# Performance work log

Measured on AMD Instinct MI355X. Metric: run time of the kernel, lower is better.

## Reference

```python
import jax, jax.numpy as jnp
import numpy as np

BATCH = 250
SEQ = 200
EMB = 100
VOCAB = 100000
UNITS = 512


def setup_inputs() -> dict:
    key = jax.random.key(0)
    ks = jax.random.split(key, 12)
    s = 0.05
    return {
        "tokens": jax.random.randint(ks[0], (BATCH, SEQ), 0, VOCAB, dtype=jnp.int64 if jax.config.jax_enable_x64 else jnp.int32),
        "emb": jax.random.normal(ks[1], (VOCAB, EMB), jnp.float32) * s,
        "k0": jax.random.normal(ks[2], (EMB, 4 * UNITS), jnp.float32) * s,
        "r0": jax.random.normal(ks[3], (UNITS, 4 * UNITS), jnp.float32) * s,
        "b0": jnp.zeros((4 * UNITS,), jnp.float32),
        "k1": jax.random.normal(ks[4], (UNITS, 4 * UNITS), jnp.float32) * s,
        "r1": jax.random.normal(ks[5], (UNITS, 4 * UNITS), jnp.float32) * s,
        "b1": jnp.zeros((4 * UNITS,), jnp.float32),
        "wd1": jax.random.normal(ks[6], (UNITS, 32), jnp.float32) * s,
        "bd1": jnp.zeros((32,), jnp.float32),
        "wd2": jax.random.normal(ks[7], (32, 1), jnp.float32) * s,
        "bd2": jnp.zeros((1,), jnp.float32),
    }


def _lstm_step(x, h, c, k, r, b):
    # Keras LSTMCell gate order: [i, f, cbar, o]
    g = x @ k + h @ r + b  # [B, 4U]
    i, f, cbar, o = jnp.split(g, 4, axis=-1)
    c_new = jax.nn.sigmoid(f) * c + jax.nn.sigmoid(i) * jnp.tanh(cbar)
    h_new = jax.nn.sigmoid(o) * jnp.tanh(c_new)
    return h_new, c_new


def reference(tokens, emb, k0, r0, b0, k1, r1, b1, wd1, bd1, wd2, bd2):
    x = emb[tokens]  # [B, T, E]
    B = x.shape[0]
    U = r0.shape[0]

    def step(carry, xt):
        h0, c0, h1, c1 = carry
        h0, c0 = _lstm_step(xt, h0, c0, k0, r0, b0)
        h1, c1 = _lstm_step(h0, h1, c1, k1, r1, b1)
        return (h0, c0, h1, c1), None

    init = tuple(jnp.zeros((B, U), x.dtype) for _ in range(4))
    (h0, c0, h1, c1), _ = jax.lax.scan(step, init, jnp.swapaxes(x, 0, 1))
    prob = jax.nn.sigmoid((h1 @ wd1 + bd1) @ wd2 + bd2)  # [B, 1]
    return prob
```

## Files before the change

kernel.cpp:

```cpp
#include <hip/hip_runtime.h>
#include <cstdint>

typedef unsigned short u16;
typedef unsigned long long u64;
typedef __attribute__((ext_vector_type(8))) short s8v;
typedef __attribute__((ext_vector_type(4))) float f4v;

#define NBLK 256
#define TSEQ 200
#define PIPE_W 8
#define HSLOT (256 * 512)

__device__ __forceinline__ u16 f2bf(float f) {
  uint32_t u = __float_as_uint(f);
  u += 0x7fffu + ((u >> 16) & 1u);
  return (u16)(u >> 16);
}
__device__ __forceinline__ float bf2f(u16 h) {
  return __uint_as_float(((uint32_t)h) << 16);
}
__device__ __forceinline__ float sigf(float x) { return 1.f / (1.f + __expf(-x)); }
__device__ __forceinline__ float tanhfast(float x) { return 2.f / (1.f + __expf(-2.f * x)) - 1.f; }

__device__ __forceinline__ void ld_c(s8v& d, const u16* p, int ofs) {
  asm volatile("global_load_dwordx4 %0, %1, off offset:%2 sc0 sc1"
               : "=v"(d) : "v"(p), "n"(ofs));
}
__device__ __forceinline__ void ld_nc(s8v& d, const u16* p, int ofs) {
  asm volatile("global_load_dwordx4 %0, %1, off offset:%2"
               : "=v"(d) : "v"(p), "n"(ofs));
}
__device__ __forceinline__ void vmwait(int n) {
  asm volatile("s_waitcnt vmcnt(%0)" :: "n"(n) : "memory");
}
__device__ __forceinline__ void cstore(u16* p, u16 v) {
  asm volatile("global_store_short %0, %1, off sc0 sc1" :: "v"(p), "v"((uint32_t)v) : "memory");
}


__global__ void zero_ws(uint32_t* p, int n) {
  int i = blockIdx.x * 256 + threadIdx.x;
  if (i < n) p[i] = 0u;
}

__global__ void gather_x(const int* __restrict__ tokens, const float* __restrict__ emb,
                         u16* __restrict__ X) {
  int idx = blockIdx.x * 256 + threadIdx.x;
  if (idx >= TSEQ * 256 * 16) return;
  int e0 = (idx & 15) * 8;
  int b  = (idx >> 4) & 255;
  int t  = idx >> 12;
  u16 v[8];
  if (b < 250) {
    int tok = tokens[b * TSEQ + t];
    const float* er = emb + (size_t)tok * 100;
#pragma unroll
    for (int j = 0; j < 8; ++j) {
      int e = e0 + j;
      v[j] = (e < 100) ? f2bf(er[e]) : (u16)0;
    }
  } else {
#pragma unroll
    for (int j = 0; j < 8; ++j) v[j] = 0;
  }
  *(s8v*)&X[(size_t)idx * 8] = *(const s8v*)v;
}

__global__ void pack_w(const float* __restrict__ A, const float* __restrict__ Bm,
                       u16* __restrict__ out, int nks, int split, int arows) {
  int idx = blockIdx.x * 256 + threadIdx.x;
  int total = 32 * nks * 256;
  if (idx >= total) return;
  int kw0 = (idx & 3) * 8;
  int col = (idx >> 2) & 63;
  int rest = idx >> 8;
  int ks = rest % nks;
  int ub = rest / nks;
  int g = col >> 4, j = col & 15;
  int oc = g * 512 + ub * 16 + j;
  u16 v[8];
#pragma unroll
  for (int w = 0; w < 8; ++w) {
    int k = ks * 32 + kw0 + w;
    float f;
    if (k < split) f = (k < arows) ? A[(size_t)k * 2048 + oc] : 0.f;
    else           f = Bm[(size_t)(k - split) * 2048 + oc];
    v[w] = f2bf(f);
  }
  int kw0s = kw0 ^ ((((col >> 1) & 3)) << 3);
  size_t dst = (((size_t)(ub * nks + ks) * 64 + col) * 32) + kw0s;
  *(s8v*)&out[dst] = *(const s8v*)v;
}


template <int NK, int S1, int S2>
__device__ __forceinline__ void pipew(const u16* p0, const u16* p1, const u16* p2,
                                      const u16* ldsW, int ldsb, f4v acc[4]) {
  s8v a[NK];
  constexpr int W = (PIPE_W < NK) ? PIPE_W : NK;
#pragma unroll
  for (int j = 0; j < W; ++j) {
    if (j < S1)      ld_nc(a[j], p0, j * 64);
    else if (j < S2) ld_c(a[j], p1, (j - S1) * 64);
    else             ld_c(a[j], p2, (j - S2) * 64);
  }
#pragma unroll
  for (int i = 0; i < NK; ++i) {
    const int j = i + W;
    if (j < NK) {
      if (j < S1)      ld_nc(a[j], p0, j * 64);
      else if (j < S2) ld_c(a[j], p1, (j - S1) * 64);
      else             ld_c(a[j], p2, (j - S2) * 64);
    }
    s8v b0 = *(const s8v*)&ldsW[i * 2048 + 0 * 512 + ldsb];
    s8v b1 = *(const s8v*)&ldsW[i * 2048 + 1 * 512 + ldsb];
    s8v b2 = *(const s8v*)&ldsW[i * 2048 + 2 * 512 + ldsb];
    s8v b3 = *(const s8v*)&ldsW[i * 2048 + 3 * 512 + ldsb];
    const int rem = NK - 1 - i;
    vmwait(W < rem ? W : rem);
    __builtin_amdgcn_sched_barrier(0);
    acc[0] = __builtin_amdgcn_mfma_f32_16x16x32_bf16(a[i], b0, acc[0], 0, 0, 0);
    acc[1] = __builtin_amdgcn_mfma_f32_16x16x32_bf16(a[i], b1, acc[1], 0, 0, 0);
    acc[2] = __builtin_amdgcn_mfma_f32_16x16x32_bf16(a[i], b2, acc[2], 0, 0, 0);
    acc[3] = __builtin_amdgcn_mfma_f32_16x16x32_bf16(a[i], b3, acc[3], 0, 0, 0);
  }
}


__global__ void __launch_bounds__(256, 1)
lstm_main(const float* __restrict__ b0, const float* __restrict__ b1,
          const u16* __restrict__ W0p, const u16* __restrict__ W1p,
          const u16* __restrict__ X, u16* __restrict__ H0,
          u16* __restrict__ H1, unsigned* __restrict__ fL0,
          unsigned* __restrict__ fL1) {
  extern __shared__ u16 lds[];
  const int tid = threadIdx.x;
  const int lane = tid & 63;
  const int w = tid >> 6;
  const int blk = blockIdx.x;
  const bool Lh = (blk >= 128);
  const int sub = blk & 127;
  const int ub = sub & 31;
  const int mt = sub >> 5;
  const int NKr = Lh ? 32 : 20;

  {
    const u16* src = (Lh ? W1p : W0p) + (size_t)ub * (NKr * 2048);
    const int total = NKr * 2048;
    for (int ofs = tid * 8; ofs < total; ofs += 2048)
      *(s8v*)&lds[ofs] = *(const s8v*)&src[ofs];
  }
  __syncthreads();

  const int colu = lane & 15;
  const int kch = (lane >> 4) * 8;
  const int kchs = kch ^ ((((colu >> 1) & 3)) << 3);
  const int arow = mt * 64 + w * 16 + colu;
  const int drow = mt * 64 + w * 16 + ((lane >> 4) << 2);
  const int ucol = ub * 16 + colu;
  const int ldsb = colu * 32 + kchs;

  unsigned* gL0 = fL0 + (mt * 4 + w) * 32;
  unsigned* gL1 = fL1 + (mt * 4 + w) * 32;
  unsigned* pollp = (lane < 32 ? gL0 : gL1) + (lane & 31);
  const int thrOfs = Lh ? (lane < 32 ? 1 : 0)
                        : (lane < 32 ? 0 : -3);
  unsigned* sigp = (Lh ? gL1 : gL0) + ub;

  float bias[4];
  {
    const float* bp = Lh ? b1 : b0;
#pragma unroll
    for (int g = 0; g < 4; ++g) bias[g] = bp[g * 512 + ucol];
  }

  float cst[4] = {0.f, 0.f, 0.f, 0.f};

  for (int t = 0; t < TSEQ; ++t) {
    const int cs = t & 3;
    const int ps = (t + 3) & 3;
    {
      const int thr = t + thrOfs;
      unsigned v;
      do {
        v = __hip_atomic_load(pollp, __ATOMIC_RELAXED, __HIP_MEMORY_SCOPE_AGENT);
      } while (!__all((int)v >= thr));
    }
    f4v acc[4] = {};
    if (!Lh) {
      const u16* ax = X + ((size_t)t * 256 + arow) * 128 + kch;
      const u16* ah = H0 + (size_t)ps * HSLOT + (size_t)arow * 512 + kch;
      pipew<20, 4, 20>(ax, ah, ah, lds, ldsb, acc);
    } else {
      const u16* ak = H0 + (size_t)cs * HSLOT + (size_t)arow * 512 + kch;
      const u16* ar = H1 + (size_t)ps * HSLOT + (size_t)arow * 512 + kch;
      pipew<32, 0, 16>(ak, ak, ar, lds, ldsb, acc);
    }
    u16* Hout = (Lh ? H1 : H0) + (size_t)cs * HSLOT;
#pragma unroll
    for (int r = 0; r < 4; ++r) {
      float gi = acc[0][r] + bias[0];
      float gf = acc[1][r] + bias[1];
      float gc = acc[2][r] + bias[2];
      float go = acc[3][r] + bias[3];
      float cn = sigf(gf) * cst[r] + sigf(gi) * tanhfast(gc);
      cst[r] = cn;
      cstore(&Hout[(size_t)(drow + r) * 512 + ucol], f2bf(sigf(go) * tanhfast(cn)));
    }
    asm volatile("s_waitcnt vmcnt(0)" ::: "memory");
    if (lane == 0)
      __hip_atomic_store(sigp, (unsigned)(t + 1), __ATOMIC_RELAXED, __HIP_MEMORY_SCOPE_AGENT);
  }
}


__global__ void dense_out(const u16* __restrict__ H1f, const float* __restrict__ wd1,
                          const float* __restrict__ bd1, const float* __restrict__ wd2,
                          const float* __restrict__ bd2, float* __restrict__ out) {
  __shared__ float wv[512];
  __shared__ float beff;
  const int t = threadIdx.x;
  {
    float s = 0.f;
#pragma unroll 4
    for (int j = 0; j < 32; ++j) s += wd1[t * 32 + j] * wd2[j];
    wv[t] = s;
  }
  if (t == 0) {
    float sb = 0.f;
    for (int j = 0; j < 32; ++j) sb += bd1[j] * wd2[j];
    beff = sb + bd2[0];
  }
  __syncthreads();
  if (t < 250) {
    const u16* hr = H1f + (size_t)t * 512;
    float acc = 0.f;
    for (int u = 0; u < 512; u += 8) {
      s8v hv = *(const s8v*)&hr[u];
#pragma unroll
      for (int j = 0; j < 8; ++j) acc += bf2f((u16)hv[j]) * wv[u + j];
    }
    out[t] = sigf(acc + beff);
  }
}


extern "C" void kernel_launch(void* const* d_in, const int* in_sizes, int n_in,
                              void* d_out, int out_size, void* d_ws, size_t ws_size,
                              hipStream_t stream) {
  const int*   tokens = (const int*)  d_in[0];
  const float* emb    = (const float*)d_in[1];
  const float* k0     = (const float*)d_in[2];
  const float* r0     = (const float*)d_in[3];
  const float* b0     = (const float*)d_in[4];
  const float* k1     = (const float*)d_in[5];
  const float* r1     = (const float*)d_in[6];
  const float* b1     = (const float*)d_in[7];
  const float* wd1    = (const float*)d_in[8];
  const float* bd1    = (const float*)d_in[9];
  const float* wd2    = (const float*)d_in[10];
  const float* bd2    = (const float*)d_in[11];
  float* out = (float*)d_out;

  char* ws = (char*)d_ws;
  unsigned* fL0 = (unsigned*)ws;
  unsigned* fL1 = (unsigned*)(ws + 2048);
  u16* H0  = (u16*)(ws + 8192);
  u16* H1  = (u16*)(ws + 8192 + 1048576);
  u16* X   = (u16*)(ws + 8192 + 2097152);
  u16* W0p = (u16*)(ws + 8192 + 2097152 + 13107200);
  u16* W1p = (u16*)(ws + 8192 + 2097152 + 13107200 + 2621440);

  zero_ws<<<2056, 256, 0, stream>>>((uint32_t*)ws, 526336);
  gather_x<<<3200, 256, 0, stream>>>(tokens, emb, X);
  pack_w<<<640,  256, 0, stream>>>(k0, r0, W0p, 20, 128, 100);
  pack_w<<<1024, 256, 0, stream>>>(k1, r1, W1p, 32, 512, 512);

  hipFuncSetAttribute(reinterpret_cast<const void*>(lstm_main),
                      hipFuncAttributeMaxDynamicSharedMemorySize, 131072);
  void* args[] = {(void*)&b0, (void*)&b1, (void*)&W0p, (void*)&W1p,
                  (void*)&X,  (void*)&H0, (void*)&H1, (void*)&fL0, (void*)&fL1};
  (void)hipLaunchCooperativeKernel(reinterpret_cast<void*>(lstm_main),
                                   dim3(NBLK), dim3(256), args, 131072, stream);

  dense_out<<<1, 512, 0, stream>>>(H1 + (size_t)3 * HSLOT, wd1, bd1, wd2, bd2, out);
}
```

Measured before the change: 2.097 ms.

## Keep LSTM weights in registers with 32x32 MFMA split-K across waves

```diff
diff --git a/kernel.cpp b/kernel.cpp
--- a/kernel.cpp
+++ b/kernel.cpp
@@ -2,13 +2,11 @@
 #include <cstdint>
 
 typedef unsigned short u16;
-typedef unsigned long long u64;
 typedef __attribute__((ext_vector_type(8))) short s8v;
 typedef __attribute__((ext_vector_type(4))) float f4v;
-
-#define NBLK 256
+typedef __attribute__((ext_vector_type(16))) float f16v;
+
 #define TSEQ 200
-#define PIPE_W 8
 #define HSLOT (256 * 512)
 
 __device__ __forceinline__ u16 f2bf(float f) {
@@ -66,151 +64,164 @@
   *(s8v*)&X[(size_t)idx * 8] = *(const s8v*)v;
 }
 
-__global__ void pack_w(const float* __restrict__ A, const float* __restrict__ Bm,
-                       u16* __restrict__ out, int nks, int split, int arows) {
+__global__ void pack_wB(const float* __restrict__ A, const float* __restrict__ Bm,
+                        u16* __restrict__ out, int nk16, int split, int arows) {
   int idx = blockIdx.x * 256 + threadIdx.x;
-  int total = 32 * nks * 256;
+  int total = 32 * nk16 * 2 * 32 * 2;
   if (idx >= total) return;
-  int kw0 = (idx & 3) * 8;
-  int col = (idx >> 2) & 63;
-  int rest = idx >> 8;
-  int ks = rest % nks;
-  int ub = rest / nks;
-  int g = col >> 4, j = col & 15;
-  int oc = g * 512 + ub * 16 + j;
+  int kh = idx & 1;
+  int col = (idx >> 1) & 31;
+  int colt = (idx >> 6) & 1;
+  int rest = idx >> 7;
+  int ks = rest % nk16;
+  int ub = rest / nk16;
+  int gcol = (colt * 2 + (col >> 4)) * 512 + ub * 16 + (col & 15);
   u16 v[8];
 #pragma unroll
-  for (int w = 0; w < 8; ++w) {
-    int k = ks * 32 + kw0 + w;
+  for (int e = 0; e < 8; ++e) {
+    int k = ks * 16 + kh * 8 + e;
     float f;
-    if (k < split) f = (k < arows) ? A[(size_t)k * 2048 + oc] : 0.f;
-    else           f = Bm[(size_t)(k - split) * 2048 + oc];
-    v[w] = f2bf(f);
-  }
-  int kw0s = kw0 ^ ((((col >> 1) & 3)) << 3);
-  size_t dst = (((size_t)(ub * nks + ks) * 64 + col) * 32) + kw0s;
-  *(s8v*)&out[dst] = *(const s8v*)v;
-}
-
-
-template <int NK, int S1, int S2>
-__device__ __forceinline__ void pipew(const u16* p0, const u16* p1, const u16* p2,
-                                      const u16* ldsW, int ldsb, f4v acc[4]) {
-  s8v a[NK];
-  constexpr int W = (PIPE_W < NK) ? PIPE_W : NK;
-#pragma unroll
-  for (int j = 0; j < W; ++j) {
-    if (j < S1)      ld_nc(a[j], p0, j * 64);
-    else if (j < S2) ld_c(a[j], p1, (j - S1) * 64);
-    else             ld_c(a[j], p2, (j - S2) * 64);
-  }
-#pragma unroll
-  for (int i = 0; i < NK; ++i) {
-    const int j = i + W;
-    if (j < NK) {
-      if (j < S1)      ld_nc(a[j], p0, j * 64);
-      else if (j < S2) ld_c(a[j], p1, (j - S1) * 64);
-      else             ld_c(a[j], p2, (j - S2) * 64);
-    }
-    s8v b0 = *(const s8v*)&ldsW[i * 2048 + 0 * 512 + ldsb];
-    s8v b1 = *(const s8v*)&ldsW[i * 2048 + 1 * 512 + ldsb];
-    s8v b2 = *(const s8v*)&ldsW[i * 2048 + 2 * 512 + ldsb];
-    s8v b3 = *(const s8v*)&ldsW[i * 2048 + 3 * 512 + ldsb];
-    const int rem = NK - 1 - i;
-    vmwait(W < rem ? W : rem);
-    __builtin_amdgcn_sched_barrier(0);
-    acc[0] = __builtin_amdgcn_mfma_f32_16x16x32_bf16(a[i], b0, acc[0], 0, 0, 0);
-    acc[1] = __builtin_amdgcn_mfma_f32_16x16x32_bf16(a[i], b1, acc[1], 0, 0, 0);
-    acc[2] = __builtin_amdgcn_mfma_f32_16x16x32_bf16(a[i], b2, acc[2], 0, 0, 0);
-    acc[3] = __builtin_amdgcn_mfma_f32_16x16x32_bf16(a[i], b3, acc[3], 0, 0, 0);
-  }
-}
-
-
-__global__ void __launch_bounds__(256, 1)
+    if (k < split) f = (k < arows) ? A[(size_t)k * 2048 + gcol] : 0.f;
+    else           f = Bm[(size_t)(k - split) * 2048 + gcol];
+    v[e] = f2bf(f);
+  }
+  *(s8v*)&out[(size_t)idx * 8] = *(const s8v*)v;
+}
+
+template <bool LH, int NS, int NK16, int NX>
+__device__ __forceinline__ void run_layer(int band, int ub, int w, int lane, int tid,
+    const u16* __restrict__ Wp, const u16* __restrict__ X,
+    u16* __restrict__ H0, u16* __restrict__ H1,
+    const float* __restrict__ bp, unsigned* fL0b, unsigned* fL1b, float* rbuf) {
+  s8v B0[NS], B1[NS];
+#pragma unroll
+  for (int s = 0; s < NS; ++s) {
+    const u16* bb = Wp + (size_t)(ub * NK16 + w * NS + s) * 1024
+                       + ((lane & 31) * 2 + (lane >> 5)) * 8;
+    B0[s] = *(const s8v*)bb;
+    B1[s] = *(const s8v*)(bb + 512);
+  }
+  const int arow = band * 32 + (lane & 31);
+  const int kchE = (lane >> 5) * 8;
+  const int u0 = (tid * 2) & 15;
+  float bias0[4], bias1[4];
+#pragma unroll
+  for (int g = 0; g < 4; ++g) {
+    bias0[g] = bp[g * 512 + ub * 16 + u0];
+    bias1[g] = bp[g * 512 + ub * 16 + u0 + 1];
+  }
+  float c0 = 0.f, c1 = 0.f;
+  unsigned* pp; int tofs;
+  if (LH) {
+    if (w < 2) { pp = fL0b + (lane & 31); tofs = 1; }
+    else       { pp = fL1b + (lane & 31); tofs = 0; }
+  } else {
+    pp = (lane < 32) ? (fL0b + lane) : (fL1b + (lane - 32));
+    tofs = (lane < 32) ? 0 : -3;
+  }
+  unsigned* sigp = (LH ? fL1b : fL0b) + ub;
+
+  for (int t = 0; t < TSEQ; ++t) {
+    const int cs = t & 3, ps = (t + 3) & 3;
+    {
+      const int thr = t + tofs;
+      unsigned v;
+      do {
+        v = __hip_atomic_load(pp, __ATOMIC_RELAXED, __HIP_MEMORY_SCOPE_AGENT);
+      } while (!__all((int)v >= thr));
+    }
+    const u16 *pH, *pX;
+    if (LH) {
+      pH = (w < 2 ? H0 + (size_t)cs * HSLOT : H1 + (size_t)ps * HSLOT)
+           + (size_t)arow * 512 + kchE + (w & 1) * 256;
+      pX = pH;
+    } else if (NX > 0) {
+      pX = X + (size_t)t * 32768 + arow * 128 + kchE;
+      pH = H0 + (size_t)ps * HSLOT + (size_t)arow * 512 + kchE - 128;
+    } else {
+      pH = H0 + (size_t)ps * HSLOT + (size_t)arow * 512 + kchE + (w * 10 - 8) * 16;
+      pX = pH;
+    }
+    f16v acc0 = {}, acc1 = {};
+    s8v a[NS];
+    constexpr int W = NS < 8 ? NS : 8;
+#pragma unroll
+    for (int s = 0; s < W; ++s) {
+      if (s < NX) ld_nc(a[s], pX, s * 32); else ld_c(a[s], pH, s * 32);
+    }
+#pragma unroll
+    for (int s = 0; s < NS; ++s) {
+      const int j = s + W;
+      if (j < NS) { if (j < NX) ld_nc(a[j], pX, j * 32); else ld_c(a[j], pH, j * 32); }
+      const int rem = NS - 1 - s;
+      vmwait(rem < W ? rem : W);
+      __builtin_amdgcn_sched_barrier(0);
+      acc0 = __builtin_amdgcn_mfma_f32_32x32x16_bf16(a[s], B0[s], acc0, 0, 0, 0);
+      acc1 = __builtin_amdgcn_mfma_f32_32x32x16_bf16(a[s], B1[s], acc1, 0, 0, 0);
+    }
+#pragma unroll
+    for (int q = 0; q < 4; ++q) {
+      f4v v0 = {acc0[4*q], acc0[4*q+1], acc0[4*q+2], acc0[4*q+3]};
+      f4v v1 = {acc1[4*q], acc1[4*q+1], acc1[4*q+2], acc1[4*q+3]};
+      *(f4v*)&rbuf[(w * 8 + q) * 256 + lane * 4] = v0;
+      *(f4v*)&rbuf[(w * 8 + 4 + q) * 256 + lane * 4] = v1;
+    }
+    __syncthreads();
+    u16* Hout = (LH ? H1 : H0) + (size_t)cs * HSLOT;
+    {
+      const int cell = tid * 2, row = cell >> 4, u = cell & 15;
+      const int hi = (row >> 2) & 1, r = (row & 3) | ((row >> 3) << 2);
+      float gs[4];
+#pragma unroll
+      for (int g = 0; g < 4; ++g) {
+        const int dwb = ((g >> 1) * 4 + (r >> 2)) * 256 + (((g & 1) << 4) + u + (hi << 5)) * 4 + (r & 3);
+        gs[g] = rbuf[dwb] + rbuf[dwb + 2048] + rbuf[dwb + 4096] + rbuf[dwb + 6144];
+      }
+      float cn = sigf(gs[1] + bias0[1]) * c0 + sigf(gs[0] + bias0[0]) * tanhfast(gs[2] + bias0[2]);
+      c0 = cn;
+      cstore(&Hout[(size_t)(band * 32 + row) * 512 + ub * 16 + u],
+             f2bf(sigf(gs[3] + bias0[3]) * tanhfast(cn)));
+    }
+    {
+      const int cell = tid * 2 + 1, row = cell >> 4, u = cell & 15;
+      const int hi = (row >> 2) & 1, r = (row & 3) | ((row >> 3) << 2);
+      float gs[4];
+#pragma unroll
+      for (int g = 0; g < 4; ++g) {
+        const int dwb = ((g >> 1) * 4 + (r >> 2)) * 256 + (((g & 1) << 4) + u + (hi << 5)) * 4 + (r & 3);
+        gs[g] = rbuf[dwb] + rbuf[dwb + 2048] + rbuf[dwb + 4096] + rbuf[dwb + 6144];
+      }
+      float cn = sigf(gs[1] + bias1[1]) * c1 + sigf(gs[0] + bias1[0]) * tanhfast(gs[2] + bias1[2]);
+      c1 = cn;
+      cstore(&Hout[(size_t)(band * 32 + row) * 512 + ub * 16 + u],
+             f2bf(sigf(gs[3] + bias1[3]) * tanhfast(cn)));
+    }
+    vmwait(0);
+    __syncthreads();
+    if (tid == 0)
+      __hip_atomic_store(sigp, (unsigned)(t + 1), __ATOMIC_RELAXED, __HIP_MEMORY_SCOPE_AGENT);
+  }
+}
+
+__global__ void __launch_bounds__(256, 2)
 lstm_main(const float* __restrict__ b0, const float* __restrict__ b1,
           const u16* __restrict__ W0p, const u16* __restrict__ W1p,
           const u16* __restrict__ X, u16* __restrict__ H0,
           u16* __restrict__ H1, unsigned* __restrict__ fL0,
           unsigned* __restrict__ fL1) {
-  extern __shared__ u16 lds[];
-  const int tid = threadIdx.x;
-  const int lane = tid & 63;
-  const int w = tid >> 6;
+  __shared__ float rbuf[8192];
+  const int tid = threadIdx.x, lane = tid & 63, w = tid >> 6;
   const int blk = blockIdx.x;
-  const bool Lh = (blk >= 128);
-  const int sub = blk & 127;
-  const int ub = sub & 31;
-  const int mt = sub >> 5;
-  const int NKr = Lh ? 32 : 20;
-
-  {
-    const u16* src = (Lh ? W1p : W0p) + (size_t)ub * (NKr * 2048);
-    const int total = NKr * 2048;
-    for (int ofs = tid * 8; ofs < total; ofs += 2048)
-      *(s8v*)&lds[ofs] = *(const s8v*)&src[ofs];
-  }
-  __syncthreads();
-
-  const int colu = lane & 15;
-  const int kch = (lane >> 4) * 8;
-  const int kchs = kch ^ ((((colu >> 1) & 3)) << 3);
-  const int arow = mt * 64 + w * 16 + colu;
-  const int drow = mt * 64 + w * 16 + ((lane >> 4) << 2);
-  const int ucol = ub * 16 + colu;
-  const int ldsb = colu * 32 + kchs;
-
-  unsigned* gL0 = fL0 + (mt * 4 + w) * 32;
-  unsigned* gL1 = fL1 + (mt * 4 + w) * 32;
-  unsigned* pollp = (lane < 32 ? gL0 : gL1) + (lane & 31);
-  const int thrOfs = Lh ? (lane < 32 ? 1 : 0)
-                        : (lane < 32 ? 0 : -3);
-  unsigned* sigp = (Lh ? gL1 : gL0) + ub;
-
-  float bias[4];
-  {
-    const float* bp = Lh ? b1 : b0;
-#pragma unroll
-    for (int g = 0; g < 4; ++g) bias[g] = bp[g * 512 + ucol];
-  }
-
-  float cst[4] = {0.f, 0.f, 0.f, 0.f};
-
-  for (int t = 0; t < TSEQ; ++t) {
-    const int cs = t & 3;
-    const int ps = (t + 3) & 3;
-    {
-      const int thr = t + thrOfs;
-      unsigned v;
-      do {
-        v = __hip_atomic_load(pollp, __ATOMIC_RELAXED, __HIP_MEMORY_SCOPE_AGENT);
-      } while (!__all((int)v >= thr));
-    }
-    f4v acc[4] = {};
-    if (!Lh) {
-      const u16* ax = X + ((size_t)t * 256 + arow) * 128 + kch;
-      const u16* ah = H0 + (size_t)ps * HSLOT + (size_t)arow * 512 + kch;
-      pipew<20, 4, 20>(ax, ah, ah, lds, ldsb, acc);
-    } else {
-      const u16* ak = H0 + (size_t)cs * HSLOT + (size_t)arow * 512 + kch;
-      const u16* ar = H1 + (size_t)ps * HSLOT + (size_t)arow * 512 + kch;
-      pipew<32, 0, 16>(ak, ak, ar, lds, ldsb, acc);
-    }
-    u16* Hout = (Lh ? H1 : H0) + (size_t)cs * HSLOT;
-#pragma unroll
-    for (int r = 0; r < 4; ++r) {
-      float gi = acc[0][r] + bias[0];
-      float gf = acc[1][r] + bias[1];
-      float gc = acc[2][r] + bias[2];
-      float go = acc[3][r] + bias[3];
-      float cn = sigf(gf) * cst[r] + sigf(gi) * tanhfast(gc);
-      cst[r] = cn;
-      cstore(&Hout[(size_t)(drow + r) * 512 + ucol], f2bf(sigf(go) * tanhfast(cn)));
-    }
-    asm volatile("s_waitcnt vmcnt(0)" ::: "memory");
-    if (lane == 0)
-      __hip_atomic_store(sigp, (unsigned)(t + 1), __ATOMIC_RELAXED, __HIP_MEMORY_SCOPE_AGENT);
-  }
+  const bool Lh = blk >= 256;
+  const int sub = blk & 255, band = sub >> 5, ub = sub & 31;
+  unsigned* fL0b = fL0 + band * 32;
+  unsigned* fL1b = fL1 + band * 32;
+  if (Lh)
+    run_layer<true, 16, 64, 0>(band, ub, w, lane, tid, W1p, X, H0, H1, b1, fL0b, fL1b, rbuf);
+  else if (w == 0)
+    run_layer<false, 10, 40, 8>(band, ub, w, lane, tid, W0p, X, H0, H1, b0, fL0b, fL1b, rbuf);
+  else
+    run_layer<false, 10, 40, 0>(band, ub, w, lane, tid, W0p, X, H0, H1, b0, fL0b, fL1b, rbuf);
 }
 
 
@@ -273,15 +284,13 @@
 
   zero_ws<<<2056, 256, 0, stream>>>((uint32_t*)ws, 526336);
   gather_x<<<3200, 256, 0, stream>>>(tokens, emb, X);
-  pack_w<<<640,  256, 0, stream>>>(k0, r0, W0p, 20, 128, 100);
-  pack_w<<<1024, 256, 0, stream>>>(k1, r1, W1p, 32, 512, 512);
-
-  hipFuncSetAttribute(reinterpret_cast<const void*>(lstm_main),
-                      hipFuncAttributeMaxDynamicSharedMemorySize, 131072);
+  pack_wB<<<640,  256, 0, stream>>>(k0, r0, W0p, 40, 128, 100);
+  pack_wB<<<1024, 256, 0, stream>>>(k1, r1, W1p, 64, 512, 512);
+
   void* args[] = {(void*)&b0, (void*)&b1, (void*)&W0p, (void*)&W1p,
                   (void*)&X,  (void*)&H0, (void*)&H1, (void*)&fL0, (void*)&fL1};
   (void)hipLaunchCooperativeKernel(reinterpret_cast<void*>(lstm_main),
-                                   dim3(NBLK), dim3(256), args, 131072, stream);
+                                   dim3(512), dim3(256), args, 0, stream);
 
   dense_out<<<1, 512, 0, stream>>>(H1 + (size_t)3 * HSLOT, wd1, bd1, wd2, bd2, out);
 }
```

Result: faster. 1.880 ms (-10.4%).
